# Performance work log

Measured on AMD Instinct MI355X. Metric: run time of the kernel, lower is better.

The kernel has to match this reference:

```python
import jax, jax.numpy as jnp
import numpy as np

EPS = 1e-7
TRUNC = 0.5          # truncation level of the robust L1 objective
K_CAND = 64          # max number of piecewise-linear extrema evaluated per row


def _pad_inf(v):
    # (B, n) -> (B, n+2) with -inf / +inf sentinels (torch _pad_inf)
    b = v.shape[0]
    return jnp.concatenate(
        [jnp.full((b, 1), -jnp.inf, v.dtype), v, jnp.full((b, 1), jnp.inf, v.dtype)], axis=-1)


def _pad_cumsum(c):
    # (B, n) -> (B, n+2): leading zero, trailing repeat of last (torch _pad_cumsum)
    return jnp.concatenate([jnp.zeros_like(c[:, :1]), c, c[:, -1:]], axis=-1)


_search_l = jax.vmap(lambda a, v: jnp.searchsorted(a, v, side='left'))
_search_r = jax.vmap(lambda a, v: jnp.searchsorted(a, v, side='right'))


def _align_trunc(x, y, w):
    # Solves min_a sum_i min(TRUNC, w_i * |a*x_i - y_i|) per row. x,y,w: (B, n).
    sign = jnp.sign(x)
    x = x * sign
    y = y * sign
    wx = w * x
    wy = w * y
    ydx = y / jnp.maximum(x, EPS)                       # breakpoints of |a x - y|
    cand_b = (wy - TRUNC) / jnp.maximum(wx, EPS)        # breakpoints where residual hits trunc
    cand_c = (wy + TRUNC) / jnp.maximum(wx, EPS)

    def sorted_cum(v):
        order = jnp.argsort(v, axis=-1)
        vs = jnp.take_along_axis(v, order, axis=-1)
        q = jnp.cumsum(jnp.take_along_axis(wx, order, axis=-1), axis=-1)
        return _pad_inf(vs), _pad_cumsum(q)

    As, QA = sorted_cum(ydx)
    Bs, QB = sorted_cum(cand_b)
    Cs, QC = sorted_cum(cand_c)

    def deriv(search):
        jA = search(As, ydx) - 1
        jB = search(Bs, ydx) - 1
        jC = search(Cs, ydx) - 1
        return (2 * jnp.take_along_axis(QA, jA, axis=-1)
                - jnp.take_along_axis(QB, jB, axis=-1)
                - jnp.take_along_axis(QC, jC, axis=-1))

    left_d = deriv(_search_l)
    right_d = deriv(_search_r)
    is_ext = (left_d < 0) & (right_d >= 0)
    is_ext = is_ext.at[:, 0].set(is_ext[:, 0] | ~jnp.any(is_ext, axis=-1))

    # first K_CAND extrema indices per row (stable sort: extrema=False-key first)
    cand_idx = jnp.argsort(~is_ext, axis=-1, stable=True)[:, :K_CAND]   # (B, K)
    valid = jnp.take_along_axis(is_ext, cand_idx, axis=-1)
    cand_a = jnp.take_along_axis(ydx, cand_idx, axis=-1)                # (B, K)

    # truncated-L1 residual at each candidate a: (B, K)
    res = jnp.sum(
        jnp.minimum(jnp.abs(cand_a[:, :, None] * x[:, None, :] - y[:, None, :]) * w[:, None, :], TRUNC),
        axis=-1)
    res = jnp.where(valid, res, jnp.inf)

    kbest = jnp.argmin(res, axis=-1)                                    # scatter_min equivalent
    loss = jnp.take_along_axis(res, kbest[:, None], axis=-1)[:, 0]
    index = jnp.take_along_axis(cand_idx, kbest[:, None], axis=-1)[:, 0]
    a = (jnp.take_along_axis(y, index[:, None], axis=-1)[:, 0]
         / jnp.maximum(jnp.take_along_axis(x, index[:, None], axis=-1)[:, 0], EPS))
    return a, loss, index


def setup_inputs() -> dict:
    key = jax.random.key(0)
    k1, k2, k3 = jax.random.split(key, 3)
    B, N = 256, 2048
    points_src = jax.random.normal(k1, (B, N, 3), dtype=jnp.float32)
    points_tgt = jax.random.normal(k2, (B, N, 3), dtype=jnp.float32)
    weight = jax.random.uniform(k3, (B, N), dtype=jnp.float32)  # weights >= 0
    return {"points_src": points_src, "points_tgt": points_tgt, "weight": weight}


def reference(points_src, points_tgt, weight):
    # align_points_scale: flatten (..., N, 3) -> (..., 3N), weight broadcast over xyz
    B = points_src.shape[0]
    x = points_src.reshape(B, -1)
    y = points_tgt.reshape(B, -1)
    w = jnp.broadcast_to(weight[..., None], points_src.shape).reshape(B, -1)
    a, loss, index = _align_trunc(x, y, w)
    return a
```

## Files before the change

### kernel.cpp

```cpp
#include <hip/hip_runtime.h>
#include <math.h>

#define NELEM   6144
#define NWEIGHT 2048
#define SORTN   8192
#define NT      1024
#define NWAVE   (NT / 64)
#define KCAND   64
#define DN      6146
#define PERT    (NELEM / NT)
#define CHUNK   (NELEM / NWAVE)
#define QSCALE  32768.0f

#define WINW     5.2e-3f
#define DELTARES 1.5e-3
#define WCAP     384

__device__ __forceinline__ int lb_spl(const float* __restrict__ key, float spl, float v) {
    int blk = 0;
#pragma unroll
    for (int st = 64; st > 0; st >>= 1) {
        int nb = blk + st;
        float p = __shfl(spl, (nb - 1) & 63);
        if (nb <= 64 && p < v) blk = nb;
    }
    int pos = blk * 96;
    const int lim = (pos + 96 < NELEM) ? (pos + 96) : NELEM;
#pragma unroll
    for (int st = 64; st > 0; st >>= 1) {
        int np = pos + st;
        if (np <= lim && key[np - 1] < v) pos = np;
    }
    return pos;
}

#define CEK(a, b, up) { float lo = fminf(K[a], K[b]), hi = fmaxf(K[a], K[b]); \
                        K[a] = (up) ? lo : hi; K[b] = (up) ? hi : lo; }

__global__ __launch_bounds__(NT, 8)
void pointloss_align_kernel(const float* __restrict__ X,
                            const float* __restrict__ Y,
                            const float* __restrict__ W,
                            float* __restrict__ out)
{
    __shared__ __align__(16) unsigned char s_mem[73744];
    float* s_sort = (float*)s_mem;
    float* s_key  = (float*)s_mem;
    int*   s_dlt  = (int*)  (s_mem + 24576);
    int*   s_dle  = (int*)  (s_mem + 49160);
    float* s_wzf  = (float*)(s_mem + 24576);
    float* s_wy2  = (float*)(s_mem + 49160);

    __shared__ int   s_wtot[2 * NWAVE];
    __shared__ int   s_woff[2 * NWAVE];
    __shared__ int   s_isum[NWAVE];
    __shared__ int   s_cand[KCAND];
    __shared__ float s_res[KCAND];
    __shared__ float s_wres[WCAP];
    __shared__ int   s_count;
    __shared__ int   s_fb;
    __shared__ float s_wa;
    __shared__ int   s_lo, s_hi;

    const int tid = threadIdx.x;
    const int row = blockIdx.x;
    const float* xb = X + (size_t)row * NELEM;
    const float* yb = Y + (size_t)row * NELEM;
    const float* wb = W + (size_t)row * NWEIGHT;

    float K[8];
    if (tid < NELEM / 8) {
        const int e0 = tid * 8;
        float4 x0 = *(const float4*)(xb + e0);
        float4 x1 = *(const float4*)(xb + e0 + 4);
        float4 y0 = *(const float4*)(yb + e0);
        float4 y1 = *(const float4*)(yb + e0 + 4);
        float xx[8] = {x0.x, x0.y, x0.z, x0.w, x1.x, x1.y, x1.z, x1.w};
        float yy[8] = {y0.x, y0.y, y0.z, y0.w, y1.x, y1.y, y1.z, y1.w};
#pragma unroll
        for (int r = 0; r < 8; ++r) {
            float x = xx[r], y = yy[r];
            float s = (x > 0.f) ? 1.f : ((x < 0.f) ? -1.f : 0.f);
            K[r] = (y * s) / fmaxf(x * s, 1e-7f);
        }
    } else {
#pragma unroll
        for (int r = 0; r < 8; ++r) K[r] = INFINITY;
    }
    if (tid == 0) s_fb = 0;

    CEK(0, 1, true); CEK(2, 3, false); CEK(4, 5, true); CEK(6, 7, false);
    CEK(0, 2, true); CEK(1, 3, true);  CEK(4, 6, false); CEK(5, 7, false);
    CEK(0, 1, true); CEK(2, 3, true);  CEK(4, 5, false); CEK(6, 7, false);
    for (int kk = 8; kk <= 512; kk <<= 1) {
        const bool up = ((tid & (kk >> 3)) == 0);
        for (int jj = kk >> 1; jj >= 8; jj >>= 1) {
            const int m = jj >> 3;
            const bool tmin = (up == ((tid & m) == 0));
#pragma unroll
            for (int r = 0; r < 8; ++r) {
                float o = __shfl_xor(K[r], m);
                K[r] = tmin ? fminf(K[r], o) : fmaxf(K[r], o);
            }
        }
        CEK(0, 4, up); CEK(1, 5, up); CEK(2, 6, up); CEK(3, 7, up);
        CEK(0, 2, up); CEK(1, 3, up); CEK(4, 6, up); CEK(5, 7, up);
        CEK(0, 1, up); CEK(2, 3, up); CEK(4, 5, up); CEK(6, 7, up);
    }
    const int xv = ((tid >> 2) & 7) << 2;
    for (int kk = 1024; kk <= SORTN; kk <<= 1) {
        {
            float4 h0 = {K[0], K[1], K[2], K[3]}, h1 = {K[4], K[5], K[6], K[7]};
            *(float4*)&s_sort[(8 * tid) ^ xv]     = h0;
            *(float4*)&s_sort[(8 * tid + 4) ^ xv] = h1;
        }
        __syncthreads();
        for (int jj = kk >> 1; jj >= 512; jj >>= 1) {
            for (int p = tid; p < SORTN / 2; p += NT) {
                const int i  = ((p & ~(jj - 1)) << 1) | (p & (jj - 1));
                const int ia = i ^ (((i >> 5) & 7) << 2);
                const int ib = ia ^ jj;
                const bool up = ((i & kk) == 0);
                float a = s_sort[ia], b = s_sort[ib];
                float lo = fminf(a, b), hi = fmaxf(a, b);
                s_sort[ia] = up ? lo : hi;
                s_sort[ib] = up ? hi : lo;
            }
            __syncthreads();
        }
        {
            float4 h0 = *(float4*)&s_sort[(8 * tid) ^ xv];
            float4 h1 = *(float4*)&s_sort[(8 * tid + 4) ^ xv];
            K[0] = h0.x; K[1] = h0.y; K[2] = h0.z; K[3] = h0.w;
            K[4] = h1.x; K[5] = h1.y; K[6] = h1.z; K[7] = h1.w;
        }
        __syncthreads();
        const bool up = ((tid & (kk >> 3)) == 0);
        for (int jj = 256; jj >= 8; jj >>= 1) {
            const int m = jj >> 3;
            const bool tmin = (up == ((tid & m) == 0));
#pragma unroll
            for (int r = 0; r < 8; ++r) {
                float o = __shfl_xor(K[r], m);
                K[r] = tmin ? fminf(K[r], o) : fmaxf(K[r], o);
            }
        }
        CEK(0, 4, up); CEK(1, 5, up); CEK(2, 6, up); CEK(3, 7, up);
        CEK(0, 2, up); CEK(1, 3, up); CEK(4, 6, up); CEK(5, 7, up);
        CEK(0, 1, up); CEK(2, 3, up); CEK(4, 5, up); CEK(6, 7, up);
    }
    if (tid < NELEM / 8) {
        float4 h0 = {K[0], K[1], K[2], K[3]}, h1 = {K[4], K[5], K[6], K[7]};
        *(float4*)&s_key[8 * tid]     = h0;
        *(float4*)&s_key[8 * tid + 4] = h1;
    }
    for (int i = tid; i < DN; i += NT) { s_dlt[i] = 0; s_dle[i] = 0; }
    __syncthreads();

    const float spl = s_key[96 * (tid & 63) + 95];

    int lvq[PERT];
    {
        const int base = tid * PERT;
#pragma unroll
        for (int q = 0; q < PERT; ++q) {
            const int j = base + q;
            float x = xb[j], y = yb[j], w = wb[j / 3];
            float s = (x > 0.f) ? 1.f : ((x < 0.f) ? -1.f : 0.f);
            float z = x * s, y2 = y * s;
            float wx = w * z, wy = w * y2;
            float mwx = fmaxf(wx, 1e-7f);
            float bbv = (wy - 0.5f) / mwx;
            float ccv = (wy + 0.5f) / mwx;
            float v = y2 / fmaxf(z, 1e-7f);
            int lv = lb_spl(s_key, spl, v);
            int uv = lv; while (uv < NELEM && s_key[uv] == v) ++uv;
            int lbp = lb_spl(s_key, spl, bbv);
            int ubp = lbp; while (ubp < NELEM && s_key[ubp] == bbv) ++ubp;
            int lcp = lb_spl(s_key, spl, ccv);
            int ucp = lcp; while (ucp < NELEM && s_key[ucp] == ccv) ++ucp;
            lvq[q] = lv;
            int qx = __float2int_rn(wx * QSCALE);
            atomicAdd(&s_dlt[uv],  2 * qx);
            atomicAdd(&s_dle[lv],  2 * qx);
            atomicAdd(&s_dlt[ubp], -qx);
            atomicAdd(&s_dle[lbp], -qx);
            atomicAdd(&s_dlt[ucp], -qx);
            atomicAdd(&s_dle[lcp], -qx);
        }
    }
    __syncthreads();

    {
        const int lane = tid & 63, wv = tid >> 6;
        const int cbase = wv * CHUNK;
        int cl = 0, ce = 0;
#pragma unroll
        for (int k = 0; k < CHUNK / 64; ++k) {
            const int p = cbase + k * 64 + lane;
            int a = s_dlt[p], b = s_dle[p];
            for (int d = 1; d < 64; d <<= 1) {
                int ua = __shfl_up(a, d);
                int ub = __shfl_up(b, d);
                if (lane >= d) { a += ua; b += ub; }
            }
            a += cl; b += ce;
            s_dlt[p] = a; s_dle[p] = b;
            cl = __shfl(a, 63); ce = __shfl(b, 63);
        }
        if (lane == 63) { s_wtot[wv] = cl; s_wtot[NWAVE + wv] = ce; }
    }
    __syncthreads();
    if (tid < NWAVE) {
        int a = s_wtot[tid], b = s_wtot[NWAVE + tid];
        const int a0 = a, b0 = b;
        for (int d = 1; d < NWAVE; d <<= 1) {
            int ua = __shfl_up(a, d);
            int ub = __shfl_up(b, d);
            if (tid >= d) { a += ua; b += ub; }
        }
        s_woff[tid] = a - a0;
        s_woff[NWAVE + tid] = b - b0;
    }
    __syncthreads();

    {
        const int base = tid * PERT;
        unsigned char fl[PERT];
        int cnt = 0;
#pragma unroll
        for (int q = 0; q < PERT; ++q) {
            const int p = lvq[q];
            const int pw = p / CHUNK;
            int L = s_dlt[p] + s_woff[pw];
            int R = s_dle[p] + s_woff[NWAVE + pw];
            bool f = (L < 0) && (R >= 0);
            fl[q] = f ? 1 : 0; cnt += fl[q];
        }
        const int lane = tid & 63, wv = tid >> 6;
        int ti = cnt;
        for (int d = 1; d < 64; d <<= 1) {
            int u = __shfl_up(ti, d);
            if (lane >= d) ti += u;
        }
        if (lane == 63) s_isum[wv] = ti;
        __syncthreads();
        int off = 0;
        for (int q = 0; q < wv; ++q) off += s_isum[q];
        const int ex = off + ti - cnt;
        if (tid == NT - 1) s_count = ex + cnt;
        int pos = ex;
#pragma unroll
        for (int q = 0; q < PERT; ++q) {
            if (fl[q]) { if (pos < KCAND) s_cand[pos] = base + q; ++pos; }
        }
    }
    __syncthreads();
    if (tid == 0 && s_count == 0) { s_cand[0] = 0; s_count = 1; s_fb = 1; }
    __syncthreads();

    for (int e = tid; e < NELEM; e += NT) {
        float x = xb[e], y = yb[e], w = wb[e / 3];
        float s = (x > 0.f) ? 1.f : ((x < 0.f) ? -1.f : 0.f);
        s_wzf[e] = w * (x * s);
        s_wy2[e] = w * (y * s);
    }
    __syncthreads();

    const int lane = tid & 63, wv = tid >> 6;
    {
        const int cnt64 = (s_count < KCAND) ? s_count : KCAND;
        for (int c = wv; c < cnt64; c += NWAVE) {
            const int j = s_cand[c];
            float x = xb[j], y = yb[j];
            float s = (x > 0.f) ? 1.f : ((x < 0.f) ? -1.f : 0.f);
            float ak = (y * s) / fmaxf(x * s, 1e-7f);
            float acc = 0.f;
            for (int e = lane; e < NELEM; e += 64)
                acc += fminf(fabsf(fmaf(ak, s_wzf[e], -s_wy2[e])), 0.5f);
            for (int d = 32; d > 0; d >>= 1) acc += __shfl_xor(acc, d);
            if (lane == 0) s_res[c] = acc;
        }
    }
    __syncthreads();
    if (tid < KCAND) {
        const int cnt64 = (s_count < KCAND) ? s_count : KCAND;
        float rv = (tid < cnt64) ? s_res[tid] : INFINITY;
        int kb = tid;
        for (int d = 32; d > 0; d >>= 1) {
            float ro = __shfl_xor(rv, d);
            int   ko = __shfl_xor(kb, d);
            if (ro < rv || (ro == rv && ko < kb)) { rv = ro; kb = ko; }
        }
        if (tid == 0) {
            const int j = s_cand[kb];
            float x = xb[j], y = yb[j];
            float s = (x > 0.f) ? 1.f : ((x < 0.f) ? -1.f : 0.f);
            s_wa = (y * s) / fmaxf(x * s, 1e-7f);
        }
    }
    __syncthreads();

    const float awin = s_wa;
    if (!s_fb) {
        int lo = lb_spl(s_key, spl, awin - WINW);
        while (lo > 0 && fabsf(s_key[lo - 1] - awin) <= WINW) --lo;
        while (lo < NELEM && fabsf(s_key[lo] - awin) > WINW) ++lo;
        int hi = lb_spl(s_key, spl, awin + WINW);
        while (hi < NELEM && fabsf(s_key[hi] - awin) <= WINW) ++hi;
        while (hi > lo && fabsf(s_key[hi - 1] - awin) > WINW) --hi;
        if (tid == 0) { s_lo = lo; s_hi = hi; }
    } else if (tid == 0) { s_lo = 0; s_hi = 0; }
    __syncthreads();
    const int lo = s_lo;
    const int wtot = s_hi - s_lo;
    const int wcnt = (wtot < WCAP) ? wtot : WCAP;
    const bool commit = (s_fb != 0) || (wtot > WCAP);
    if (!commit) {
        for (int c = wv; c < wcnt; c += NWAVE) {
            float ak = s_key[lo + c];
            float acc = 0.f;
            for (int e = lane; e < NELEM; e += 64)
                acc += fminf(fabsf(fmaf(ak, s_wzf[e], -s_wy2[e])), 0.5f);
            for (int d = 32; d > 0; d >>= 1) acc += __shfl_xor(acc, d);
            if (lane == 0) s_wres[c] = acc;
        }
    }
    __syncthreads();

    if (tid == 0) {
        float outv = awin;
        if (!commit && wcnt > 0) {
            double rmin = INFINITY;
            for (int i = 0; i < wcnt; ++i) rmin = fmin(rmin, (double)s_wres[i]);
            double A = INFINITY, B = -INFINITY;
            for (int i = 0; i < wcnt; ++i) {
                double excess = (double)s_wres[i] - rmin;
                if (excess <= DELTARES) {
                    double a = (double)s_key[lo + i];
                    A = fmin(A, a + excess);
                    B = fmax(B, a - excess);
                }
            }
            outv = (float)(0.5 * (A + B));
        }
        out[row] = outv;
    }
}

extern "C" void kernel_launch(void* const* d_in, const int* in_sizes, int n_in,
                              void* d_out, int out_size, void* d_ws, size_t ws_size,
                              hipStream_t stream) {
    const float* X = (const float*)d_in[0];
    const float* Y = (const float*)d_in[1];
    const float* W = (const float*)d_in[2];
    float* out = (float*)d_out;
    const int nrows = in_sizes[0] / NELEM;
    pointloss_align_kernel<<<dim3(nrows), dim3(NT), 0, stream>>>(X, Y, W, out);
}
```

Baseline: 105.0 us.

## Interleave weighted x/y in LDS and evaluate four candidates per wave pass

Stores the weighted x and y values as interleaved float2 pairs in shared memory, so each lane reads two elements with a single float4 load. Each wave now evaluates the truncated-L1 residual for four candidate slopes per sweep over the data instead of one. This cuts LDS traffic and loop overhead by reusing each loaded element across four candidates. The trade-offs are more accumulator registers and possible idle waves when the candidate count is not a multiple of four.

After: 96.74 us. -7.8%, faster.

```diff
diff --git a/kernel.cpp b/kernel.cpp
--- a/kernel.cpp
+++ b/kernel.cpp
@@ -34,6 +34,29 @@
     return pos;
 }
 
+__device__ __forceinline__ void res_eval4(const float4* __restrict__ wq, int lane,
+                                          const float* __restrict__ ak,
+                                          float* __restrict__ r) {
+    float c0 = 0.f, c1 = 0.f, c2 = 0.f, c3 = 0.f;
+#pragma unroll 1
+    for (int k = 0; k < NELEM / 128; ++k) {
+        float4 q = wq[(k << 6) + lane];
+        c0 += fminf(fabsf(fmaf(ak[0], q.x, -q.y)), 0.5f);
+        c1 += fminf(fabsf(fmaf(ak[1], q.x, -q.y)), 0.5f);
+        c2 += fminf(fabsf(fmaf(ak[2], q.x, -q.y)), 0.5f);
+        c3 += fminf(fabsf(fmaf(ak[3], q.x, -q.y)), 0.5f);
+        c0 += fminf(fabsf(fmaf(ak[0], q.z, -q.w)), 0.5f);
+        c1 += fminf(fabsf(fmaf(ak[1], q.z, -q.w)), 0.5f);
+        c2 += fminf(fabsf(fmaf(ak[2], q.z, -q.w)), 0.5f);
+        c3 += fminf(fabsf(fmaf(ak[3], q.z, -q.w)), 0.5f);
+    }
+    for (int d = 32; d > 0; d >>= 1) {
+        c0 += __shfl_xor(c0, d); c1 += __shfl_xor(c1, d);
+        c2 += __shfl_xor(c2, d); c3 += __shfl_xor(c3, d);
+    }
+    r[0] = c0; r[1] = c1; r[2] = c2; r[3] = c3;
+}
+
 #define CEK(a, b, up) { float lo = fminf(K[a], K[b]), hi = fmaxf(K[a], K[b]); \
                         K[a] = (up) ? lo : hi; K[b] = (up) ? hi : lo; }
 
@@ -44,12 +67,12 @@
                             float* __restrict__ out)
 {
     __shared__ __align__(16) unsigned char s_mem[73744];
-    float* s_sort = (float*)s_mem;
-    float* s_key  = (float*)s_mem;
-    int*   s_dlt  = (int*)  (s_mem + 24576);
-    int*   s_dle  = (int*)  (s_mem + 49160);
-    float* s_wzf  = (float*)(s_mem + 24576);
-    float* s_wy2  = (float*)(s_mem + 49160);
+    float*  s_sort = (float*)s_mem;
+    float*  s_key  = (float*)s_mem;
+    int*    s_dlt  = (int*)  (s_mem + 24576);
+    int*    s_dle  = (int*)  (s_mem + 49160);
+    float2* s_wq2  = (float2*)(s_mem + 24576);
+    const float4* s_wq4 = (const float4*)(s_mem + 24576);
 
     __shared__ int   s_wtot[2 * NWAVE];
     __shared__ int   s_woff[2 * NWAVE];
@@ -262,24 +285,34 @@
     for (int e = tid; e < NELEM; e += NT) {
         float x = xb[e], y = yb[e], w = wb[e / 3];
         float s = (x > 0.f) ? 1.f : ((x < 0.f) ? -1.f : 0.f);
-        s_wzf[e] = w * (x * s);
-        s_wy2[e] = w * (y * s);
+        float2 p; p.x = w * (x * s); p.y = w * (y * s);
+        s_wq2[e] = p;
     }
     __syncthreads();
 
     const int lane = tid & 63, wv = tid >> 6;
     {
         const int cnt64 = (s_count < KCAND) ? s_count : KCAND;
-        for (int c = wv; c < cnt64; c += NWAVE) {
-            const int j = s_cand[c];
-            float x = xb[j], y = yb[j];
-            float s = (x > 0.f) ? 1.f : ((x < 0.f) ? -1.f : 0.f);
-            float ak = (y * s) / fmaxf(x * s, 1e-7f);
-            float acc = 0.f;
-            for (int e = lane; e < NELEM; e += 64)
-                acc += fminf(fabsf(fmaf(ak, s_wzf[e], -s_wy2[e])), 0.5f);
-            for (int d = 32; d > 0; d >>= 1) acc += __shfl_xor(acc, d);
-            if (lane == 0) s_res[c] = acc;
+        const int c0 = 4 * wv;
+        if (c0 < cnt64) {
+            float ak[4];
+#pragma unroll
+            for (int q = 0; q < 4; ++q) {
+                int c = c0 + q;
+                if (c < cnt64) {
+                    const int j = s_cand[c];
+                    float x = xb[j], y = yb[j];
+                    float s = (x > 0.f) ? 1.f : ((x < 0.f) ? -1.f : 0.f);
+                    ak[q] = (y * s) / fmaxf(x * s, 1e-7f);
+                } else ak[q] = 0.f;
+            }
+            float r[4];
+            res_eval4(s_wq4, lane, ak, r);
+            if (lane == 0) {
+#pragma unroll
+                for (int q = 0; q < 4; ++q)
+                    if (c0 + q < cnt64) s_res[c0 + q] = r[q];
+            }
         }
     }
     __syncthreads();
@@ -317,13 +350,20 @@
     const int wcnt = (wtot < WCAP) ? wtot : WCAP;
     const bool commit = (s_fb != 0) || (wtot > WCAP);
     if (!commit) {
-        for (int c = wv; c < wcnt; c += NWAVE) {
-            float ak = s_key[lo + c];
-            float acc = 0.f;
-            for (int e = lane; e < NELEM; e += 64)
-                acc += fminf(fabsf(fmaf(ak, s_wzf[e], -s_wy2[e])), 0.5f);
-            for (int d = 32; d > 0; d >>= 1) acc += __shfl_xor(acc, d);
-            if (lane == 0) s_wres[c] = acc;
+        for (int cb = 4 * wv; cb < wcnt; cb += 64) {
+            float ak[4];
+#pragma unroll
+            for (int q = 0; q < 4; ++q) {
+                int c = cb + q;
+                ak[q] = (c < wcnt) ? s_key[lo + c] : 0.f;
+            }
+            float r[4];
+            res_eval4(s_wq4, lane, ak, r);
+            if (lane == 0) {
+#pragma unroll
+                for (int q = 0; q < 4; ++q)
+                    if (cb + q < wcnt) s_wres[cb + q] = r[q];
+            }
         }
     }
     __syncthreads();
```
